# Kernel optimization log

Measured on AMD Instinct MI355X. Metric: run time of the kernel, lower is better.

The kernel has to match this reference:

```python
import jax, jax.numpy as jnp
import numpy as np

B, H, L, D = 2, 16, 2048, 64


def setup_inputs() -> dict:
    key = jax.random.key(0)
    ks = jax.random.split(key, 5)
    q = jax.random.normal(ks[0], (B, H, L, D), dtype=jnp.float32)
    k = jax.random.normal(ks[1], (B, H, L, D), dtype=jnp.float32)
    v = jax.random.normal(ks[2], (B, H, L, D), dtype=jnp.float32)
    pe_q = jax.random.normal(ks[3], (B, H, L, D), dtype=jnp.float32)
    pe_k = jax.random.normal(ks[4], (B, H, L, D), dtype=jnp.float32)
    # causal mask, broadcast over batch: True = keep
    mask = jnp.broadcast_to(jnp.tril(jnp.ones((L, L), dtype=bool)), (B, L, L))
    return {"q": q, "k": k, "v": v, "pe_q": pe_q, "pe_k": pe_k, "mask": mask}


def reference(q, k, v, pe_q, pe_k, mask):
    scale = q.shape[-1] ** (-0.5)
    # dual-score: content QK^T + positional PE_Q PE_K^T, fused before softmax
    attn = (jnp.einsum('bhqd,bhkd->bhqk', q, k)
            + jnp.einsum('bhqd,bhkd->bhqk', pe_q, pe_k)) * scale
    # mask: [B, L, L] -> [B, 1, L, L]; False positions get -inf
    attn = jnp.where(mask[:, None, :, :], attn, -jnp.inf)
    attn = jax.nn.softmax(attn, axis=-1)
    return jnp.einsum('bhqk,bhkd->bhqd', attn, v)
```

## Files before the change

### kernel.cpp

```cpp
#include <hip/hip_runtime.h>
#include <hip/hip_bf16.h>


typedef unsigned short u16;
typedef unsigned int   u32;
typedef __attribute__((ext_vector_type(8))) short bf16x8;
typedef __attribute__((ext_vector_type(4))) float f32x4;

#define L_SEQ 2048
#define D_DIM 64
#define BQ    64
#define BK    32
#define NQT   (L_SEQ / BQ)

__device__ __forceinline__ float bf2f(u32 lo16) {
    u32 u = lo16 << 16; float f; __builtin_memcpy(&f, &u, 4); return f;
}

__global__ void detect_dtype_kernel(const u16* __restrict__ q, int* __restrict__ flag) {
    const int lane = threadIdx.x;
    float x = fabsf(bf2f((u32)q[lane]));
    bool big = !(x <= 100.f);
    unsigned long long m = __ballot(big);
    if (lane == 0) *flag = (m != 0ull) ? 1 : 0;
}

__device__ __forceinline__ void split_pack(const float* x, uint4& h, uint4& l) {
    u32 xb[8], rb[8];
#pragma unroll
    for (int j = 0; j < 8; ++j) {
        __builtin_memcpy(&xb[j], &x[j], 4);
        u32 hb = xb[j] & 0xffff0000u;
        float hf; __builtin_memcpy(&hf, &hb, 4);
        float r = x[j] - hf;
        __builtin_memcpy(&rb[j], &r, 4);
    }
    h.x = (xb[0] >> 16) | (xb[1] & 0xffff0000u);
    h.y = (xb[2] >> 16) | (xb[3] & 0xffff0000u);
    h.z = (xb[4] >> 16) | (xb[5] & 0xffff0000u);
    h.w = (xb[6] >> 16) | (xb[7] & 0xffff0000u);
    l.x = (rb[0] >> 16) | (rb[1] & 0xffff0000u);
    l.y = (rb[2] >> 16) | (rb[3] & 0xffff0000u);
    l.z = (rb[4] >> 16) | (rb[5] & 0xffff0000u);
    l.w = (rb[6] >> 16) | (rb[7] & 0xffff0000u);
}

template<bool IS_F32>
__device__ __forceinline__ void unpack8(const uint4& a, const uint4& b, float* x) {
    if (IS_F32) {
        u32 w[8] = {a.x, a.y, a.z, a.w, b.x, b.y, b.z, b.w};
#pragma unroll
        for (int j = 0; j < 8; ++j) __builtin_memcpy(&x[j], &w[j], 4);
    } else {
        u32 w[4] = {a.x, a.y, a.z, a.w};
#pragma unroll
        for (int j = 0; j < 4; ++j) {
            x[2*j]   = bf2f(w[j] & 0xffffu);
            x[2*j+1] = bf2f(w[j] >> 16);
        }
    }
}

struct StKE { uint4 k0, k1, e0, e1; };
struct StV  { u32 v[8]; };

template<bool IS_F32>
__device__ __forceinline__ void issue_ke(const void* Kv, const void* Ev,
        size_t base, int kbase, int r, int j8, StKE& R) {
    const size_t off = base + (size_t)(kbase + r) * D_DIM + j8 * 8;
    if (IS_F32) {
        const uint4* kp = (const uint4*)((const float*)Kv + off);
        R.k0 = kp[0]; R.k1 = kp[1];
        const uint4* ep = (const uint4*)((const float*)Ev + off);
        R.e0 = ep[0]; R.e1 = ep[1];
    } else {
        R.k0 = *(const uint4*)((const u16*)Kv + off);
        R.e0 = *(const uint4*)((const u16*)Ev + off);
    }
}

template<bool IS_F32>
__device__ __forceinline__ void issue_v(const void* Vv,
        size_t base, int kbase, int d, int kg, StV& R) {
    const size_t off = base + (size_t)(kbase + kg * 8) * D_DIM + d;
    if (IS_F32) {
        const u32* vp = (const u32*)((const float*)Vv + off);
#pragma unroll
        for (int j = 0; j < 8; ++j) R.v[j] = vp[j * D_DIM];
    } else {
        const u16* vp = (const u16*)Vv + off;
#pragma unroll
        for (int j = 0; j < 8; ++j) R.v[j] = (u32)vp[j * D_DIM];
    }
}

#define MFMA(a, b, c) __builtin_amdgcn_mfma_f32_16x16x32_bf16((a), (b), (c), 0, 0, 0)

template<bool IS_F32>
__global__ __launch_bounds__(512, 4) void attn_pair(
    const void* __restrict__ Qv, const void* __restrict__ Kv,
    const void* __restrict__ Vv, const void* __restrict__ PQv,
    const void* __restrict__ PKv, void* __restrict__ Ov,
    const int* __restrict__ flag)
{
    if (((*flag) != 0) != IS_F32) return;

    const int bh   = blockIdx.y;
    const int qa   = ((int)blockIdx.x + bh) & 15;
    const int t    = threadIdx.x;
    const int w    = t >> 6;
    const int lane = t & 63;
    const int g    = lane >> 4;
    const int c    = lane & 15;
    const size_t base = (size_t)bh * L_SEQ * D_DIM;
    const int qtile = (w < 4) ? qa : (31 - qa);
    const int qb_w  = qtile * BQ + (w & 3) * 16;
    const int nkt   = 64 - 2 * qa;

    __shared__ __align__(16) u16 Kt[BK * 128];
    __shared__ __align__(16) u16 Et[BK * 128];
    __shared__ __align__(16) u16 Vt[32 * 128];
    __shared__ __align__(16) u16 Pb[8][8 * 128];

    bf16x8 qa_h[4], qa_l[4];
    {
        const int qrow = qb_w + c;
#pragma unroll
        for (int ch = 0; ch < 4; ++ch) {
            const void* src = (ch < 2) ? Qv : PQv;
            const int d0 = (ch & 1) * 32 + 8 * g;
            const size_t off = base + (size_t)qrow * D_DIM + d0;
            float x[8];
            if (IS_F32) {
                const uint4* gp = (const uint4*)((const float*)src + off);
                unpack8<true>(gp[0], gp[1], x);
            } else {
                uint4 a = *(const uint4*)((const u16*)src + off);
                unpack8<false>(a, a, x);
            }
#pragma unroll
            for (int j = 0; j < 8; ++j) x[j] *= 0.125f;
            uint4 hp, lp; split_pack(x, hp, lp);
            u32 hw[4] = {hp.x, hp.y, hp.z, hp.w}, lw[4] = {lp.x, lp.y, lp.z, lp.w};
#pragma unroll
            for (int j = 0; j < 4; ++j) {
                qa_h[ch][2*j]   = (short)(hw[j] & 0xffffu);
                qa_h[ch][2*j+1] = (short)(hw[j] >> 16);
                qa_l[ch][2*j]   = (short)(lw[j] & 0xffffu);
                qa_l[ch][2*j+1] = (short)(lw[j] >> 16);
            }
        }
    }

    float mr[4], lr[4];
    f32x4 acc[4];
#pragma unroll
    for (int i = 0; i < 4; ++i) { mr[i] = -INFINITY; lr[i] = 0.f; }
#pragma unroll
    for (int df = 0; df < 4; ++df) acc[df] = (f32x4){0.f, 0.f, 0.f, 0.f};

    const bool is_ke = (t < 256);
    const int ts   = t & 255;
    const int r_t  = ts >> 3;
    const int j8_t = ts & 7;
    const int d_t  = ts & 63;
    const int kg_t = (ts >> 6) & 3;
    const int ke_wo = r_t * 128 + (j8_t ^ (r_t & 7)) * 8;
    const int v_rr  = d_t >> 1;
    const int v_wo  = v_rr * 128 + ((4 * (d_t & 1) + kg_t) ^ (v_rr & 7)) * 8;

    StKE Rke; StV Rv;
    if (is_ke) issue_ke<IS_F32>(Kv, PKv, base, 0, r_t, j8_t, Rke);
    else       issue_v <IS_F32>(Vv, base, 0, d_t, kg_t, Rv);

    for (int kt = 0; kt < nkt; ++kt) {
        const int kbase = kt * BK;
        __syncthreads();
        if (is_ke) {
            float x[8]; uint4 hp, lp;
            unpack8<IS_F32>(Rke.k0, Rke.k1, x);
            split_pack(x, hp, lp);
            *(uint4*)(Kt + ke_wo)      = hp;
            *(uint4*)(Kt + ke_wo + 64) = lp;
            unpack8<IS_F32>(Rke.e0, Rke.e1, x);
            split_pack(x, hp, lp);
            *(uint4*)(Et + ke_wo)      = hp;
            *(uint4*)(Et + ke_wo + 64) = lp;
        } else {
            float x[8]; uint4 hp, lp;
#pragma unroll
            for (int j = 0; j < 8; ++j) {
                if (IS_F32) __builtin_memcpy(&x[j], &Rv.v[j], 4);
                else        x[j] = bf2f(Rv.v[j]);
            }
            split_pack(x, hp, lp);
            *(uint4*)(Vt + v_wo)      = hp;
            *(uint4*)(Vt + v_wo + 64) = lp;
        }
        __syncthreads();

        if (kt + 1 < nkt) {
            if (is_ke) issue_ke<IS_F32>(Kv, PKv, base, kbase + BK, r_t, j8_t, Rke);
            else       issue_v <IS_F32>(Vv, base, kbase + BK, d_t, kg_t, Rv);
        }

        if (kbase <= qb_w + 15) {
            const bool do1 = (kbase + 16 <= qb_w + 15);
            const int c7 = c & 7;
            f32x4 s0 = {0,0,0,0}, s1 = {0,0,0,0};
#pragma unroll
            for (int ch = 0; ch < 4; ++ch) {
                const u16* Bp = (ch < 2) ? Kt : Et;
                const int sh = ((((ch & 1) * 4 + g) ^ c7)) * 8;
                const u16* r0 = Bp + c * 128;
                bf16x8 b0h = *(const bf16x8*)(r0 + sh);
                bf16x8 b0l = *(const bf16x8*)(r0 + sh + 64);
                s0 = MFMA(qa_h[ch], b0h, s0);
                s0 = MFMA(qa_h[ch], b0l, s0);
                s0 = MFMA(qa_l[ch], b0h, s0);
                if (do1) {
                    const u16* r1 = Bp + (c + 16) * 128;
                    bf16x8 b1h = *(const bf16x8*)(r1 + sh);
                    bf16x8 b1l = *(const bf16x8*)(r1 + sh + 64);
                    s1 = MFMA(qa_h[ch], b1h, s1);
                    s1 = MFMA(qa_h[ch], b1l, s1);
                    s1 = MFMA(qa_l[ch], b1h, s1);
                }
            }
#pragma unroll
            for (int i = 0; i < 4; ++i) {
                const int r = qb_w + 4 * g + i;
                if (kbase + c > r)                s0[i] = -INFINITY;
                if (!do1 || kbase + 16 + c > r)   s1[i] = -INFINITY;
            }
            float vm[4];
#pragma unroll
            for (int i = 0; i < 4; ++i) vm[i] = fmaxf(s0[i], s1[i]);
#pragma unroll
            for (int off = 1; off < 16; off <<= 1) {
#pragma unroll
                for (int i = 0; i < 4; ++i) vm[i] = fmaxf(vm[i], __shfl_xor(vm[i], off));
            }
            float al[4];
#pragma unroll
            for (int i = 0; i < 4; ++i) {
                float mn = fmaxf(mr[i], vm[i]);
                al[i] = __expf(mr[i] - mn);
                mr[i] = mn;
            }
            f32x4 p0, p1;
#pragma unroll
            for (int i = 0; i < 4; ++i) {
                p0[i] = __expf(s0[i] - mr[i]);
                p1[i] = __expf(s1[i] - mr[i]);
            }
            float rs[4];
#pragma unroll
            for (int i = 0; i < 4; ++i) rs[i] = p0[i] + p1[i];
#pragma unroll
            for (int off = 1; off < 16; off <<= 1) {
#pragma unroll
                for (int i = 0; i < 4; ++i) rs[i] += __shfl_xor(rs[i], off);
            }
#pragma unroll
            for (int i = 0; i < 4; ++i) lr[i] = lr[i] * al[i] + rs[i];
#pragma unroll
            for (int df = 0; df < 4; ++df) {
#pragma unroll
                for (int i = 0; i < 4; ++i) acc[df][i] *= al[i];
            }
            u16* pp = (u16*)Pb[w];
#pragma unroll
            for (int i = 0; i < 4; ++i) {
                const int rrp = 2 * g + (i >> 1);
                const int sb  = 4 * (i & 1);
                const int h3  = rrp & 7;
                u16* rowp = pp + rrp * 128 + c7;
                const float x0 = p0[i];
                const float x1 = p1[i];
                u32 b0; __builtin_memcpy(&b0, &x0, 4);
                u32 h0 = b0 & 0xffff0000u; float h0f; __builtin_memcpy(&h0f, &h0, 4);
                float l0f = x0 - h0f; u32 l0; __builtin_memcpy(&l0, &l0f, 4);
                u32 b1; __builtin_memcpy(&b1, &x1, 4);
                u32 h1 = b1 & 0xffff0000u; float h1f; __builtin_memcpy(&h1f, &h1, 4);
                float l1f = x1 - h1f; u32 l1; __builtin_memcpy(&l1, &l1f, 4);
                const int s0i = (sb + (c >> 3)) ^ h3;
                const int s1i = (sb + 2 + (c >> 3)) ^ h3;
                rowp[s0i * 8]       = (u16)(b0 >> 16);
                rowp[(8 + s0i) * 8] = (u16)(l0 >> 16);
                rowp[s1i * 8]       = (u16)(b1 >> 16);
                rowp[(8 + s1i) * 8] = (u16)(l1 >> 16);
            }
            const int sv = ((4 * (c & 1) + g) ^ ((c >> 1) & 7)) * 8;
            const u16* pw = pp + (c >> 1) * 128;
            bf16x8 pa_h = *(const bf16x8*)(pw + sv);
            bf16x8 pa_l = *(const bf16x8*)(pw + sv + 64);
#pragma unroll
            for (int df = 0; df < 4; ++df) {
                const u16* vw = Vt + (8 * df + (c >> 1)) * 128;
                bf16x8 vbh = *(const bf16x8*)(vw + sv);
                bf16x8 vbl = *(const bf16x8*)(vw + sv + 64);
                acc[df] = MFMA(pa_h, vbh, acc[df]);
                acc[df] = MFMA(pa_h, vbl, acc[df]);
                acc[df] = MFMA(pa_l, vbh, acc[df]);
            }
        }
    }

    float inv[4];
#pragma unroll
    for (int i = 0; i < 4; ++i) inv[i] = 1.f / lr[i];
    if (IS_F32) {
        float* o = (float*)Ov + base;
#pragma unroll
        for (int df = 0; df < 4; ++df)
#pragma unroll
            for (int i = 0; i < 4; ++i)
                o[(size_t)(qb_w + 4 * g + i) * D_DIM + 16 * df + c] = acc[df][i] * inv[i];
    } else {
        __hip_bfloat16* o = (__hip_bfloat16*)Ov + base;
#pragma unroll
        for (int df = 0; df < 4; ++df)
#pragma unroll
            for (int i = 0; i < 4; ++i)
                o[(size_t)(qb_w + 4 * g + i) * D_DIM + 16 * df + c] =
                    __float2bfloat16(acc[df][i] * inv[i]);
    }
}

extern "C" void kernel_launch(void* const* d_in, const int* in_sizes, int n_in,
                              void* d_out, int out_size, void* d_ws, size_t ws_size,
                              hipStream_t stream) {
    const void* q  = d_in[0];
    const void* k  = d_in[1];
    const void* v  = d_in[2];
    const void* pq = d_in[3];
    const void* pk = d_in[4];
    int* flag = (int*)d_ws;

    detect_dtype_kernel<<<1, 64, 0, stream>>>((const u16*)q, flag);

    dim3 grid(NQT / 2, 32);
    attn_pair<false><<<grid, 512, 0, stream>>>(q, k, v, pq, pk, d_out, flag);
    attn_pair<true ><<<grid, 512, 0, stream>>>(q, k, v, pq, pk, d_out, flag);
}
```

Baseline: 304.2 us.

## Double-buffer K/E/V tiles, transpose score MFMA, pass P via shuffles

```diff
diff --git a/kernel.cpp b/kernel.cpp
--- a/kernel.cpp
+++ b/kernel.cpp
@@ -117,10 +117,9 @@
     const int qb_w  = qtile * BQ + (w & 3) * 16;
     const int nkt   = 64 - 2 * qa;
 
-    __shared__ __align__(16) u16 Kt[BK * 128];
-    __shared__ __align__(16) u16 Et[BK * 128];
-    __shared__ __align__(16) u16 Vt[32 * 128];
-    __shared__ __align__(16) u16 Pb[8][8 * 128];
+    __shared__ __align__(16) u16 Kt[2][BK * 128];
+    __shared__ __align__(16) u16 Et[2][BK * 128];
+    __shared__ __align__(16) u16 Vt[2][32 * 128];
 
     bf16x8 qa_h[4], qa_l[4];
     {
@@ -152,10 +151,8 @@
         }
     }
 
-    float mr[4], lr[4];
+    float mr = -INFINITY, lr = 0.f;
     f32x4 acc[4];
-#pragma unroll
-    for (int i = 0; i < 4; ++i) { mr[i] = -INFINITY; lr[i] = 0.f; }
 #pragma unroll
     for (int df = 0; df < 4; ++df) acc[df] = (f32x4){0.f, 0.f, 0.f, 0.f};
 
@@ -170,22 +167,18 @@
     const int v_wo  = v_rr * 128 + ((4 * (d_t & 1) + kg_t) ^ (v_rr & 7)) * 8;
 
     StKE Rke; StV Rv;
-    if (is_ke) issue_ke<IS_F32>(Kv, PKv, base, 0, r_t, j8_t, Rke);
-    else       issue_v <IS_F32>(Vv, base, 0, d_t, kg_t, Rv);
-
-    for (int kt = 0; kt < nkt; ++kt) {
-        const int kbase = kt * BK;
-        __syncthreads();
+
+    auto stage_store = [&](int b) {
         if (is_ke) {
             float x[8]; uint4 hp, lp;
             unpack8<IS_F32>(Rke.k0, Rke.k1, x);
             split_pack(x, hp, lp);
-            *(uint4*)(Kt + ke_wo)      = hp;
-            *(uint4*)(Kt + ke_wo + 64) = lp;
+            *(uint4*)(&Kt[b][0] + ke_wo)      = hp;
+            *(uint4*)(&Kt[b][0] + ke_wo + 64) = lp;
             unpack8<IS_F32>(Rke.e0, Rke.e1, x);
             split_pack(x, hp, lp);
-            *(uint4*)(Et + ke_wo)      = hp;
-            *(uint4*)(Et + ke_wo + 64) = lp;
+            *(uint4*)(&Et[b][0] + ke_wo)      = hp;
+            *(uint4*)(&Et[b][0] + ke_wo + 64) = lp;
         } else {
             float x[8]; uint4 hp, lp;
 #pragma unroll
@@ -194,110 +187,123 @@
                 else        x[j] = bf2f(Rv.v[j]);
             }
             split_pack(x, hp, lp);
-            *(uint4*)(Vt + v_wo)      = hp;
-            *(uint4*)(Vt + v_wo + 64) = lp;
-        }
-        __syncthreads();
+            *(uint4*)(&Vt[b][0] + v_wo)      = hp;
+            *(uint4*)(&Vt[b][0] + v_wo + 64) = lp;
+        }
+    };
+    auto issue = [&](int kbase) {
+        if (is_ke) issue_ke<IS_F32>(Kv, PKv, base, kbase, r_t, j8_t, Rke);
+        else       issue_v <IS_F32>(Vv, base, kbase, d_t, kg_t, Rv);
+    };
+
+    issue(0);
+    stage_store(0);
+    issue(BK);
+    __syncthreads();
+
+    const int c7 = c & 7;
+    const int srcA = 32 * (g & 1) + c;
+    const int srcB = srcA + 16;
+
+    for (int kt = 0; kt < nkt; ++kt) {
+        const int cur = kt & 1;
+        const int kbase = kt * BK;
 
         if (kt + 1 < nkt) {
-            if (is_ke) issue_ke<IS_F32>(Kv, PKv, base, kbase + BK, r_t, j8_t, Rke);
-            else       issue_v <IS_F32>(Vv, base, kbase + BK, d_t, kg_t, Rv);
+            stage_store(cur ^ 1);
+            if (kt + 2 < nkt) issue(kbase + 2 * BK);
         }
 
         if (kbase <= qb_w + 15) {
             const bool do1 = (kbase + 16 <= qb_w + 15);
-            const int c7 = c & 7;
+            const u16* Ktc = &Kt[cur][0];
+            const u16* Etc = &Et[cur][0];
+            const u16* Vtc = &Vt[cur][0];
             f32x4 s0 = {0,0,0,0}, s1 = {0,0,0,0};
 #pragma unroll
             for (int ch = 0; ch < 4; ++ch) {
-                const u16* Bp = (ch < 2) ? Kt : Et;
+                const u16* Bp = (ch < 2) ? Ktc : Etc;
                 const int sh = ((((ch & 1) * 4 + g) ^ c7)) * 8;
                 const u16* r0 = Bp + c * 128;
                 bf16x8 b0h = *(const bf16x8*)(r0 + sh);
                 bf16x8 b0l = *(const bf16x8*)(r0 + sh + 64);
-                s0 = MFMA(qa_h[ch], b0h, s0);
-                s0 = MFMA(qa_h[ch], b0l, s0);
-                s0 = MFMA(qa_l[ch], b0h, s0);
+                s0 = MFMA(b0h, qa_h[ch], s0);
+                s0 = MFMA(b0l, qa_h[ch], s0);
+                s0 = MFMA(b0h, qa_l[ch], s0);
                 if (do1) {
                     const u16* r1 = Bp + (c + 16) * 128;
                     bf16x8 b1h = *(const bf16x8*)(r1 + sh);
                     bf16x8 b1l = *(const bf16x8*)(r1 + sh + 64);
-                    s1 = MFMA(qa_h[ch], b1h, s1);
-                    s1 = MFMA(qa_h[ch], b1l, s1);
-                    s1 = MFMA(qa_l[ch], b1h, s1);
+                    s1 = MFMA(b1h, qa_h[ch], s1);
+                    s1 = MFMA(b1l, qa_h[ch], s1);
+                    s1 = MFMA(b1h, qa_l[ch], s1);
                 }
             }
+            const int qrow = qb_w + c;
 #pragma unroll
             for (int i = 0; i < 4; ++i) {
-                const int r = qb_w + 4 * g + i;
-                if (kbase + c > r)                s0[i] = -INFINITY;
-                if (!do1 || kbase + 16 + c > r)   s1[i] = -INFINITY;
-            }
-            float vm[4];
-#pragma unroll
-            for (int i = 0; i < 4; ++i) vm[i] = fmaxf(s0[i], s1[i]);
-#pragma unroll
-            for (int off = 1; off < 16; off <<= 1) {
-#pragma unroll
-                for (int i = 0; i < 4; ++i) vm[i] = fmaxf(vm[i], __shfl_xor(vm[i], off));
-            }
-            float al[4];
+                if (kbase + 4 * g + i > qrow)                s0[i] = -INFINITY;
+                if (!do1 || kbase + 16 + 4 * g + i > qrow)   s1[i] = -INFINITY;
+            }
+            float vm = fmaxf(fmaxf(fmaxf(s0[0], s0[1]), fmaxf(s0[2], s0[3])),
+                             fmaxf(fmaxf(s1[0], s1[1]), fmaxf(s1[2], s1[3])));
+            vm = fmaxf(vm, __shfl_xor(vm, 16));
+            vm = fmaxf(vm, __shfl_xor(vm, 32));
+            const float mn = fmaxf(mr, vm);
+            const float al = __expf(mr - mn);
+            mr = mn;
+            float p0f[4], p1f[4];
 #pragma unroll
             for (int i = 0; i < 4; ++i) {
-                float mn = fmaxf(mr[i], vm[i]);
-                al[i] = __expf(mr[i] - mn);
-                mr[i] = mn;
-            }
-            f32x4 p0, p1;
+                p0f[i] = __expf(s0[i] - mn);
+                p1f[i] = __expf(s1[i] - mn);
+            }
+            float rs = (p0f[0] + p0f[1]) + (p0f[2] + p0f[3])
+                     + (p1f[0] + p1f[1]) + (p1f[2] + p1f[3]);
+            rs += __shfl_xor(rs, 16);
+            rs += __shfl_xor(rs, 32);
+            lr = lr * al + rs;
+            float al4[4];
+#pragma unroll
+            for (int i = 0; i < 4; ++i) al4[i] = __shfl(al, 20 * g + i);
+#pragma unroll
+            for (int df = 0; df < 4; ++df) {
+#pragma unroll
+                for (int i = 0; i < 4; ++i) acc[df][i] *= al4[i];
+            }
+            u32 w0[4], w1[4];
 #pragma unroll
             for (int i = 0; i < 4; ++i) {
-                p0[i] = __expf(s0[i] - mr[i]);
-                p1[i] = __expf(s1[i] - mr[i]);
-            }
-            float rs[4];
-#pragma unroll
-            for (int i = 0; i < 4; ++i) rs[i] = p0[i] + p1[i];
-#pragma unroll
-            for (int off = 1; off < 16; off <<= 1) {
-#pragma unroll
-                for (int i = 0; i < 4; ++i) rs[i] += __shfl_xor(rs[i], off);
-            }
-#pragma unroll
-            for (int i = 0; i < 4; ++i) lr[i] = lr[i] * al[i] + rs[i];
-#pragma unroll
-            for (int df = 0; df < 4; ++df) {
-#pragma unroll
-                for (int i = 0; i < 4; ++i) acc[df][i] *= al[i];
-            }
-            u16* pp = (u16*)Pb[w];
-#pragma unroll
-            for (int i = 0; i < 4; ++i) {
-                const int rrp = 2 * g + (i >> 1);
-                const int sb  = 4 * (i & 1);
-                const int h3  = rrp & 7;
-                u16* rowp = pp + rrp * 128 + c7;
-                const float x0 = p0[i];
-                const float x1 = p1[i];
+                const float x0 = p0f[i];
                 u32 b0; __builtin_memcpy(&b0, &x0, 4);
                 u32 h0 = b0 & 0xffff0000u; float h0f; __builtin_memcpy(&h0f, &h0, 4);
                 float l0f = x0 - h0f; u32 l0; __builtin_memcpy(&l0, &l0f, 4);
+                w0[i] = (b0 >> 16) | (l0 & 0xffff0000u);
+                const float x1 = p1f[i];
                 u32 b1; __builtin_memcpy(&b1, &x1, 4);
                 u32 h1 = b1 & 0xffff0000u; float h1f; __builtin_memcpy(&h1f, &h1, 4);
                 float l1f = x1 - h1f; u32 l1; __builtin_memcpy(&l1, &l1f, 4);
-                const int s0i = (sb + (c >> 3)) ^ h3;
-                const int s1i = (sb + 2 + (c >> 3)) ^ h3;
-                rowp[s0i * 8]       = (u16)(b0 >> 16);
-                rowp[(8 + s0i) * 8] = (u16)(l0 >> 16);
-                rowp[s1i * 8]       = (u16)(b1 >> 16);
-                rowp[(8 + s1i) * 8] = (u16)(l1 >> 16);
-            }
-            const int sv = ((4 * (c & 1) + g) ^ ((c >> 1) & 7)) * 8;
-            const u16* pw = pp + (c >> 1) * 128;
-            bf16x8 pa_h = *(const bf16x8*)(pw + sv);
-            bf16x8 pa_l = *(const bf16x8*)(pw + sv + 64);
+                w1[i] = (b1 >> 16) | (l1 & 0xffff0000u);
+            }
+            const bool lowhalf = (lane < 32);
+            bf16x8 pa_h, pa_l;
+#pragma unroll
+            for (int i = 0; i < 4; ++i) {
+                u32 t0a = (u32)__shfl((int)w0[i], srcA);
+                u32 t1a = (u32)__shfl((int)w1[i], srcA);
+                u32 t0b = (u32)__shfl((int)w0[i], srcB);
+                u32 t1b = (u32)__shfl((int)w1[i], srcB);
+                u32 ha = lowhalf ? t0a : t1a;
+                u32 hb = lowhalf ? t0b : t1b;
+                pa_h[i]     = (short)(ha & 0xffffu);
+                pa_h[4 + i] = (short)(hb & 0xffffu);
+                pa_l[i]     = (short)(ha >> 16);
+                pa_l[4 + i] = (short)(hb >> 16);
+            }
 #pragma unroll
             for (int df = 0; df < 4; ++df) {
-                const u16* vw = Vt + (8 * df + (c >> 1)) * 128;
+                const int sv = ((4 * (c & 1) + g) ^ ((c >> 1) & 7)) * 8;
+                const u16* vw = Vtc + (8 * df + (c >> 1)) * 128;
                 bf16x8 vbh = *(const bf16x8*)(vw + sv);
                 bf16x8 vbl = *(const bf16x8*)(vw + sv + 64);
                 acc[df] = MFMA(pa_h, vbh, acc[df]);
@@ -305,11 +311,12 @@
                 acc[df] = MFMA(pa_l, vbh, acc[df]);
             }
         }
+        __syncthreads();
     }
 
     float inv[4];
 #pragma unroll
-    for (int i = 0; i < 4; ++i) inv[i] = 1.f / lr[i];
+    for (int i = 0; i < 4; ++i) inv[i] = 1.f / __shfl(lr, 20 * g + i);
     if (IS_F32) {
         float* o = (float*)Ov + base;
 #pragma unroll
```

Result: faster. 265.6 us (-12.7%).
